# Optimization experiments

Hardware: AMD Instinct MI355X
Metric: run time of the kernel (lower is better)

The kernel has to match this reference:

```python
import jax, jax.numpy as jnp
import numpy as np

N, E = 100000, 1600000
IN, H, OUT = 64, 64, 32
BN_EPS = 1e-5


def setup_inputs() -> dict:
    key = jax.random.key(0)
    ks = jax.random.split(key, 13)

    def w(k, shape, fan_in):
        return jax.random.uniform(k, shape, jnp.float32, -1.0, 1.0) / np.sqrt(fan_in)

    return {
        "x": jax.random.normal(ks[0], (N, IN), jnp.float32),
        "edge_index": jax.random.randint(ks[1], (2, E), 0, N, jnp.int32),
        "W1": w(ks[2], (IN, H), IN),
        "b1": jnp.zeros((H,), jnp.float32),
        "gamma": jnp.ones((H,), jnp.float32),
        "beta": jnp.zeros((H,), jnp.float32),
        "W2": w(ks[3], (H, H), H),
        "b2": jnp.zeros((H,), jnp.float32),
        "lin2_w": w(ks[4], (H, OUT), H),
        "lin2_b": w(ks[5], (OUT,), H),
        "lin3_w": w(ks[6], (OUT, H), OUT),
        "lin3_b": w(ks[7], (H,), OUT),
    }


def gcn_conv(x, src, dst, W, b):
    # PyG GCNConv: h = D^{-1/2} (A + I) D^{-1/2} (x W) + b
    n = x.shape[0]
    h = x @ W  # [N, H]
    loop = jnp.arange(n, dtype=src.dtype)
    s = jnp.concatenate([src, loop])  # add self-loops
    d = jnp.concatenate([dst, loop])
    deg = jax.ops.segment_sum(jnp.ones_like(s, x.dtype), d, num_segments=n)
    dinv = jnp.where(deg > 0, jax.lax.rsqrt(deg), 0.0)
    norm = dinv[s] * dinv[d]  # [E+N]
    msg = h[s] * norm[:, None]  # gather + scale
    out = jax.ops.segment_sum(msg, d, num_segments=n)  # scatter-add
    return out + b


def reference(x, edge_index, W1, b1, gamma, beta, W2, b2, lin2_w, lin2_b, lin3_w, lin3_b):
    src, dst = edge_index[0], edge_index[1]
    h = gcn_conv(x, src, dst, W1, b1)
    # BatchNorm1d in eval mode with default running stats (mean=0, var=1)
    h = gamma * (h * jax.lax.rsqrt(jnp.float32(1.0 + BN_EPS))) + beta
    h = jax.nn.relu(h)  # dropout is identity in eval
    h = gcn_conv(h, src, dst, W2, b2)
    logits = h @ lin2_w + lin2_b  # [N, OUT]
    p = jax.nn.softmax(logits, axis=-1)
    ent = -jnp.sum(p * jnp.log(p + 1e-9), axis=-1)  # [N]
    wts = 1.0 / (ent + 1e-10)
    wts = (wts - wts.min()) / (wts.max() - wts.min())
    wts = jax.nn.softmax(wts, axis=0)  # [N]
    graph = jnp.sum(logits * wts[:, None], axis=0, keepdims=True)  # [1, OUT]
    return graph @ lin3_w + lin3_b  # [1, H]
```

## Files before the change

kernel.cpp:

```cpp
#include <hip/hip_runtime.h>
#include <hip/hip_bf16.h>
#include <hip/hip_fp8.h>
#include <math.h>


#define F 64
#define OUTF 32
#define PB 128
#define LEDGE 5632
#define WG 512
#define C1S 24
#define BN_INV 0.9999950000374997f
#define ESC_X 32.0f
#define IESC_X 0.03125f
#define ESC_Z 64.0f
#define IESC_Z 0.015625f

typedef short bf16x8 __attribute__((ext_vector_type(8)));
typedef float f32x4 __attribute__((ext_vector_type(4)));
typedef const __attribute__((address_space(1))) void* gas_ptr;
typedef __attribute__((address_space(3))) void* las_ptr;

__device__ __forceinline__ unsigned short f2bf(float f) {
    unsigned u = __float_as_uint(f);
    return (unsigned short)((u + 0x7fffu + ((u >> 16) & 1u)) >> 16);
}
__device__ __forceinline__ float bf2f(unsigned short h) {
    return __uint_as_float((unsigned)h << 16);
}

#if __has_builtin(__builtin_amdgcn_cvt_f32_fp8) && __has_builtin(__builtin_amdgcn_cvt_pk_fp8_f32)
__device__ __forceinline__ float4 fp8x4(unsigned v) {
    return make_float4(__builtin_amdgcn_cvt_f32_fp8((int)v, 0),
                       __builtin_amdgcn_cvt_f32_fp8((int)v, 1),
                       __builtin_amdgcn_cvt_f32_fp8((int)v, 2),
                       __builtin_amdgcn_cvt_f32_fp8((int)v, 3));
}
__device__ __forceinline__ unsigned fp8pk4(float a, float b, float c, float d) {
    int r = __builtin_amdgcn_cvt_pk_fp8_f32(a, b, 0, false);
    r = __builtin_amdgcn_cvt_pk_fp8_f32(c, d, r, true);
    return (unsigned)r;
}
__device__ __forceinline__ unsigned char fp8enc1(float a) {
    return (unsigned char)(__builtin_amdgcn_cvt_pk_fp8_f32(a, a, 0, false) & 0xff);
}
#else
__device__ __forceinline__ float fp8d1(unsigned char b) {
    __hip_fp8_e4m3 v; v.__x = (__hip_fp8_storage_t)b; return (float)v;
}
__device__ __forceinline__ float4 fp8x4(unsigned v) {
    return make_float4(fp8d1(v & 255u), fp8d1((v >> 8) & 255u), fp8d1((v >> 16) & 255u), fp8d1((v >> 24) & 255u));
}
__device__ __forceinline__ unsigned char fp8enc1(float a) {
    return (unsigned char)__hip_fp8_e4m3(a).__x;
}
__device__ __forceinline__ unsigned fp8pk4(float a, float b, float c, float d) {
    return (unsigned)fp8enc1(a) | ((unsigned)fp8enc1(b) << 8) | ((unsigned)fp8enc1(c) << 16) | ((unsigned)fp8enc1(d) << 24);
}
#endif

__device__ __forceinline__ void scan_btot(const int* __restrict__ btot, int* sbase, int NBK, int tid) {
    if (tid < 64) {
        int lane = tid;
        int vals[8];
        int lsum = 0;
#pragma unroll
        for (int q = 0; q < 8; q++) {
            int idx = lane * 8 + q;
            int v = (idx < NBK) ? btot[idx] : 0;
            vals[q] = lsum;
            lsum += v;
        }
        int run = lsum;
        for (int off = 1; off < 64; off <<= 1) {
            int u = __shfl_up(run, off, 64);
            if (lane >= off) run += u;
        }
        int excl = run - lsum;
#pragma unroll
        for (int q = 0; q < 8; q++) {
            int idx = lane * 8 + q;
            if (idx <= NBK) sbase[idx] = excl + vals[q];
        }
        if (lane == 63) sbase[NBK] = run;
    }
    __syncthreads();
}

__global__ __launch_bounds__(256) void k_hist(const int* __restrict__ dst, int* __restrict__ hist,
                                              int E, int NBK,
                                              const float* __restrict__ W1, const float* __restrict__ b1,
                                              const float* __restrict__ gamma, const float* __restrict__ beta,
                                              const float* __restrict__ W2, const float* __restrict__ b2,
                                              const float* __restrict__ l2w, const float* __restrict__ l2b,
                                              unsigned short* __restrict__ w1f, unsigned short* __restrict__ w2f,
                                              float* __restrict__ bias1f, float* __restrict__ b2l2) {
    __shared__ int lh[512];
    int t = threadIdx.x, blk = blockIdx.x;
    if (blk >= PB) {
        int tt = (blk - PB) * 256 + t;
        int k = tt >> 5, cc = tt & 31;
        float o = 0.0f;
        for (int j = 0; j < F; j++) o += W2[k * F + j] * l2w[j * OUTF + cc];
        {
            int t2 = cc >> 4, s = k >> 5, kb = (k >> 3) & 3, jj = k & 7;
            int ln = kb * 16 + (cc & 15);
            w2f[(size_t)((t2 * 2 + s) * 64 + ln) * 8 + jj] = f2bf(o);
        }
        for (int e = tt; e < F * F; e += 2048) {
            int kk = e >> 6, c = e & 63;
            float wv = W1[kk * F + c] * gamma[c] * BN_INV;
            int t1i = c >> 4, s = kk >> 5, kb = (kk >> 3) & 3, jj = kk & 7;
            int ln = kb * 16 + (c & 15);
            w1f[(size_t)((t1i * 2 + s) * 64 + ln) * 8 + jj] = f2bf(wv);
        }
        if (tt < F) bias1f[tt] = fmaf(b1[tt], gamma[tt] * BN_INV, beta[tt]);
        if (tt < OUTF) {
            float b = l2b[tt];
            for (int j = 0; j < F; j++) b += b2[j] * l2w[j * OUTF + tt];
            b2l2[tt] = b;
        }
        return;
    }
    for (int b = t; b < NBK; b += 256) lh[b] = 0;
    __syncthreads();
    int chunk = (E + PB - 1) / PB;
    int beg = blk * chunk, end = min(beg + chunk, E);
    for (int e = beg + t; e < end; e += 256) atomicAdd(&lh[dst[e] >> 8], 1);
    __syncthreads();
    for (int b = t; b < NBK; b += 256) hist[blk * NBK + b] = lh[b];
}

__global__ __launch_bounds__(PB) void k_hscan1(int* __restrict__ hist, int* __restrict__ btot, int NBK) {
    __shared__ int s[PB];
    int b = blockIdx.x, t = threadIdx.x;
    int v = hist[t * NBK + b];
    s[t] = v;
    __syncthreads();
    for (int off = 1; off < PB; off <<= 1) {
        int u = (t >= off) ? s[t - off] : 0;
        __syncthreads();
        s[t] += u;
        __syncthreads();
    }
    hist[t * NBK + b] = s[t] - v;
    if (t == PB - 1) btot[b] = s[t];
}

__global__ __launch_bounds__(256) void k_place(const int* __restrict__ src, const int* __restrict__ dst,
                                               const int* __restrict__ hist, const int* __restrict__ btot,
                                               unsigned* __restrict__ bucketArr, int E, int NBK) {
    __shared__ int cur[512];
    __shared__ int sbase[513];
    int t = threadIdx.x, blk = blockIdx.x;
    scan_btot(btot, sbase, NBK, t);
    for (int b = t; b < NBK; b += 256) cur[b] = hist[blk * NBK + b] + sbase[b];
    __syncthreads();
    int chunk = (E + PB - 1) / PB;
    int beg = blk * chunk, end = min(beg + chunk, E);
    for (int e = beg + t; e < end; e += 256) {
        int d = dst[e], sidx = src[e];
        int p = atomicAdd(&cur[d >> 8], 1);
        bucketArr[p] = ((unsigned)sidx << 8) | (unsigned)(d & 255);
    }
}

__global__ __launch_bounds__(256) void k_binsort(const unsigned* __restrict__ bucketArr,
                                                 const int* __restrict__ btot,
                                                 int* __restrict__ eidx, int4* __restrict__ meta,
                                                 const float4* __restrict__ x4, unsigned* __restrict__ xq, int N, int NBK) {
    __shared__ unsigned ledge[LEDGE];
    __shared__ int lcnt[256], lofs[256], lcur[256], lscan[256];
    __shared__ int sbase[513];
    __shared__ float ldinv[256];
    int b = blockIdx.x, t = threadIdx.x;
    scan_btot(btot, sbase, NBK, t);
    int gb = sbase[b];
    int count = min(sbase[b + 1] - gb, LEDGE);
    for (int j = t; j < count; j += 256) ledge[j] = bucketArr[gb + j];
    lcnt[t] = 0;
    __syncthreads();
    for (int j = t; j < count; j += 256) atomicAdd(&lcnt[ledge[j] & 255u], 1);
    __syncthreads();
    int deg = lcnt[t];
    lscan[t] = deg;
    __syncthreads();
    for (int off = 1; off < 256; off <<= 1) {
        int u = (t >= off) ? lscan[t - off] : 0;
        __syncthreads();
        lscan[t] += u;
        __syncthreads();
    }
    lofs[t] = lscan[t] - deg;
    lcur[t] = 0;
    int node = (b << 8) + t;
    float di = rsqrtf((float)deg + 1.0f);
    ldinv[t] = di;
    if (node < N) meta[node] = make_int4(gb + lofs[t], deg, __float_as_int(di), 0);
    __syncthreads();
    for (int j = t; j < count; j += 256) {
        unsigned v = ledge[j];
        int loc = (int)(v & 255u);
        int p = atomicAdd(&lcur[loc], 1);
        eidx[gb + lofs[loc] + p] = (int)(v >> 8);
    }
    for (int idx = t; idx < 256 * 16; idx += 256) {
        int nd = (b << 8) + (idx >> 4);
        if (nd < N) {
            float d2 = ldinv[idx >> 4] * ESC_X;
            float4 v = x4[(size_t)nd * 16 + (idx & 15)];
            xq[(size_t)nd * 16 + (idx & 15)] = fp8pk4(v.x * d2, v.y * d2, v.z * d2, v.w * d2);
        }
    }
}

__global__ __launch_bounds__(128) void k_c1z(const char* __restrict__ xqc,
                                             const int4* __restrict__ meta,
                                             const int* __restrict__ eidx,
                                             const unsigned short* __restrict__ w1f,
                                             const unsigned short* __restrict__ w2f,
                                             const float* __restrict__ bias1f,
                                             unsigned char* __restrict__ z2q, int N, int Em1) {
    __shared__ __align__(16) unsigned char stage[2][C1S][64 * 16];
    __shared__ __align__(16) unsigned short tile[2][16][72];
    __shared__ float ldin[2][16];
    int tid = threadIdx.x, wave = tid >> 6, lane = tid & 63;
    int g = lane >> 2, gl = lane & 3, gbase = lane & 60;
    int i = (blockIdx.x * 2 + wave) * 16 + g;
    int ic = min(i, N - 1);
    int4 m = meta[ic];
    int beg = m.x;
    int dcnt = (i < N) ? m.y : 0;
    float dis = __int_as_float(m.z) * IESC_X;
    if (gl == 0) ldin[wave][g] = __int_as_float(m.z);
    int s0 = eidx[min(beg + gl, Em1)];
    int s1 = eidx[min(beg + 4 + gl, Em1)];
    int s2 = eidx[min(beg + 8 + gl, Em1)];
    int s3 = eidx[min(beg + 12 + gl, Em1)];
    int s4 = eidx[min(beg + 16 + gl, Em1)];
    int s5 = eidx[min(beg + 20 + gl, Em1)];
    uint4 selfv = *(const uint4*)(xqc + (size_t)ic * 64 + gl * 16);
#pragma unroll
    for (int k = 0; k < C1S; k++) {
        int sreg = (k < 4) ? s0 : (k < 8) ? s1 : (k < 12) ? s2 : (k < 16) ? s3 : (k < 20) ? s4 : s5;
        int sv = __shfl(sreg, gbase + (k & 3), 64);
        if (k < dcnt) {
            const void* gp = xqc + (size_t)sv * 64 + gl * 16;
            __builtin_amdgcn_global_load_lds((gas_ptr)gp, (las_ptr)&stage[wave][k][0], 16, 0, 0);
        }
    }
    int cl = lane & 15, kb = lane >> 4;
    const bf16x8* w1v = (const bf16x8*)w1f;
    const bf16x8* w2v = (const bf16x8*)w2f;
    bf16x8 w1frag[8];
#pragma unroll
    for (int q = 0; q < 8; q++) w1frag[q] = w1v[q * 64 + lane];
    bf16x8 w2frag[4];
#pragma unroll
    for (int q = 0; q < 4; q++) w2frag[q] = w2v[q * 64 + lane];
    float bias_t[4];
#pragma unroll
    for (int t = 0; t < 4; t++) bias_t[t] = bias1f[t * 16 + cl];
    float4 a0 = fp8x4(selfv.x), a1 = fp8x4(selfv.y), a2 = fp8x4(selfv.z), a3 = fp8x4(selfv.w);
    asm volatile("s_waitcnt vmcnt(0)" ::: "memory");
#pragma unroll
    for (int k = 0; k < C1S; k++) {
        if (k < dcnt) {
            uint4 v = *(const uint4*)&stage[wave][k][lane * 16];
            float4 vA = fp8x4(v.x), vB = fp8x4(v.y), vC = fp8x4(v.z), vD = fp8x4(v.w);
            a0.x += vA.x; a0.y += vA.y; a0.z += vA.z; a0.w += vA.w;
            a1.x += vB.x; a1.y += vB.y; a1.z += vB.z; a1.w += vB.w;
            a2.x += vC.x; a2.y += vC.y; a2.z += vC.z; a2.w += vC.w;
            a3.x += vD.x; a3.y += vD.y; a3.z += vD.z; a3.w += vD.w;
        }
    }
    for (int base = C1S; base < dcnt; base += 4) {
        int j = base + gl;
        int ss = eidx[min(beg + j, Em1)];
        int cnt = min(dcnt - base, 4);
#pragma unroll
        for (int k = 0; k < 4; k++) {
            if (k < cnt) {
                int sv = __shfl(ss, gbase + k, 64);
                uint4 v = *(const uint4*)(xqc + (size_t)sv * 64 + gl * 16);
                float4 vA = fp8x4(v.x), vB = fp8x4(v.y), vC = fp8x4(v.z), vD = fp8x4(v.w);
                a0.x += vA.x; a0.y += vA.y; a0.z += vA.z; a0.w += vA.w;
                a1.x += vB.x; a1.y += vB.y; a1.z += vB.z; a1.w += vB.w;
                a2.x += vC.x; a2.y += vC.y; a2.z += vC.z; a2.w += vC.w;
                a3.x += vD.x; a3.y += vD.y; a3.z += vD.z; a3.w += vD.w;
            }
        }
    }
    {
        uint4 o1, o2;
        o1.x = (unsigned)f2bf(a0.x * dis) | ((unsigned)f2bf(a0.y * dis) << 16);
        o1.y = (unsigned)f2bf(a0.z * dis) | ((unsigned)f2bf(a0.w * dis) << 16);
        o1.z = (unsigned)f2bf(a1.x * dis) | ((unsigned)f2bf(a1.y * dis) << 16);
        o1.w = (unsigned)f2bf(a1.z * dis) | ((unsigned)f2bf(a1.w * dis) << 16);
        o2.x = (unsigned)f2bf(a2.x * dis) | ((unsigned)f2bf(a2.y * dis) << 16);
        o2.y = (unsigned)f2bf(a2.z * dis) | ((unsigned)f2bf(a2.w * dis) << 16);
        o2.z = (unsigned)f2bf(a3.x * dis) | ((unsigned)f2bf(a3.y * dis) << 16);
        o2.w = (unsigned)f2bf(a3.z * dis) | ((unsigned)f2bf(a3.w * dis) << 16);
        uint4* tp = (uint4*)&tile[wave][g][gl * 16];
        tp[0] = o1;
        tp[1] = o2;
    }
    bf16x8 af0 = *(const bf16x8*)&tile[wave][cl][kb * 8];
    bf16x8 af1 = *(const bf16x8*)&tile[wave][cl][32 + kb * 8];
    f32x4 acc[4] = {};
#pragma unroll
    for (int t = 0; t < 4; t++) {
        acc[t] = __builtin_amdgcn_mfma_f32_16x16x32_bf16(af0, w1frag[t * 2 + 0], acc[t], 0, 0, 0);
        acc[t] = __builtin_amdgcn_mfma_f32_16x16x32_bf16(af1, w1frag[t * 2 + 1], acc[t], 0, 0, 0);
    }
    float di[4];
#pragma unroll
    for (int j = 0; j < 4; j++) di[j] = ldin[wave][kb * 4 + j];
#pragma unroll
    for (int t = 0; t < 4; t++)
#pragma unroll
        for (int j = 0; j < 4; j++) {
            float h = fmaxf(acc[t][j] + bias_t[t], 0.0f) * di[j];
            tile[wave][kb * 4 + j][t * 16 + cl] = f2bf(h);
        }
    bf16x8 h0 = *(const bf16x8*)&tile[wave][cl][kb * 8];
    bf16x8 h1 = *(const bf16x8*)&tile[wave][cl][32 + kb * 8];
    f32x4 accz[2] = {};
#pragma unroll
    for (int t2 = 0; t2 < 2; t2++) {
        accz[t2] = __builtin_amdgcn_mfma_f32_16x16x32_bf16(h0, w2frag[t2 * 2 + 0], accz[t2], 0, 0, 0);
        accz[t2] = __builtin_amdgcn_mfma_f32_16x16x32_bf16(h1, w2frag[t2 * 2 + 1], accz[t2], 0, 0, 0);
    }
    int row0 = (blockIdx.x * 2 + wave) * 16;
#pragma unroll
    for (int t2 = 0; t2 < 2; t2++)
#pragma unroll
        for (int j = 0; j < 4; j++) {
            int r = row0 + kb * 4 + j;
            if (r < N) z2q[(size_t)r * OUTF + t2 * 16 + cl] = fp8enc1(accz[t2][j] * ESC_Z);
        }
}

__device__ __forceinline__ void conv2_consume(const uint2 (&vbuf)[24], uint2 selfv, int dcnt,
                                              int i, int beg, float dis, int gl, int gbase,
                                              const uint2* __restrict__ z2q2, const int* __restrict__ eidx,
                                              int Em1, float4 bvA, float4 bvB,
                                              unsigned short* __restrict__ logits_bf,
                                              float* __restrict__ wraw,
                                              float& mnW, float& mxW, int N) {
    float4 aA0 = fp8x4(selfv.x), aB0 = fp8x4(selfv.y);
    if (i >= N) { aA0 = make_float4(0.f, 0.f, 0.f, 0.f); aB0 = aA0; }
    float4 aA1 = make_float4(0.f, 0.f, 0.f, 0.f), aB1 = aA1;
#pragma unroll
    for (int k = 0; k < 24; k++) {
        if (k < dcnt) {
            float4 vA = fp8x4(vbuf[k].x), vB = fp8x4(vbuf[k].y);
            if (k & 1) {
                aA1.x += vA.x; aA1.y += vA.y; aA1.z += vA.z; aA1.w += vA.w;
                aB1.x += vB.x; aB1.y += vB.y; aB1.z += vB.z; aB1.w += vB.w;
            } else {
                aA0.x += vA.x; aA0.y += vA.y; aA0.z += vA.z; aA0.w += vA.w;
                aB0.x += vB.x; aB0.y += vB.y; aB0.z += vB.z; aB0.w += vB.w;
            }
        }
    }
    for (int base = 24; base < dcnt; base += 4) {
        int j = base + gl;
        int ss = eidx[min(beg + j, Em1)];
        int cnt = min(dcnt - base, 4);
#pragma unroll
        for (int k = 0; k < 4; k++) {
            if (k < cnt) {
                int sv = __shfl(ss, gbase + k, 64);
                uint2 v = z2q2[(size_t)sv * 4 + gl];
                float4 vA = fp8x4(v.x), vB = fp8x4(v.y);
                aA0.x += vA.x; aA0.y += vA.y; aA0.z += vA.z; aA0.w += vA.w;
                aB0.x += vB.x; aB0.y += vB.y; aB0.z += vB.z; aB0.w += vB.w;
            }
        }
    }
    float4 lgA, lgB;
    lgA.x = fmaf(aA0.x + aA1.x, dis, bvA.x);
    lgA.y = fmaf(aA0.y + aA1.y, dis, bvA.y);
    lgA.z = fmaf(aA0.z + aA1.z, dis, bvA.z);
    lgA.w = fmaf(aA0.w + aA1.w, dis, bvA.w);
    lgB.x = fmaf(aB0.x + aB1.x, dis, bvB.x);
    lgB.y = fmaf(aB0.y + aB1.y, dis, bvB.y);
    lgB.z = fmaf(aB0.z + aB1.z, dis, bvB.z);
    lgB.w = fmaf(aB0.w + aB1.w, dis, bvB.w);
    if (i < N) {
        uint4 ob;
        ob.x = (unsigned)f2bf(lgA.x) | ((unsigned)f2bf(lgA.y) << 16);
        ob.y = (unsigned)f2bf(lgA.z) | ((unsigned)f2bf(lgA.w) << 16);
        ob.z = (unsigned)f2bf(lgB.x) | ((unsigned)f2bf(lgB.y) << 16);
        ob.w = (unsigned)f2bf(lgB.z) | ((unsigned)f2bf(lgB.w) << 16);
        *(uint4*)(logits_bf + (size_t)i * OUTF + gl * 8) = ob;
    }
    float m8 = fmaxf(fmaxf(fmaxf(lgA.x, lgA.y), fmaxf(lgA.z, lgA.w)),
                     fmaxf(fmaxf(lgB.x, lgB.y), fmaxf(lgB.z, lgB.w)));
    for (int off = 2; off > 0; off >>= 1) m8 = fmaxf(m8, __shfl_xor(m8, off, 4));
    float p0 = __expf(lgA.x - m8), p1 = __expf(lgA.y - m8), p2 = __expf(lgA.z - m8), p3 = __expf(lgA.w - m8);
    float p4 = __expf(lgB.x - m8), p5 = __expf(lgB.y - m8), p6 = __expf(lgB.z - m8), p7 = __expf(lgB.w - m8);
    float s8 = p0 + p1 + p2 + p3 + p4 + p5 + p6 + p7;
    for (int off = 2; off > 0; off >>= 1) s8 += __shfl_xor(s8, off, 4);
    float inv = 1.0f / s8;
    float t0 = p0 * inv, t1v = p1 * inv, t2v = p2 * inv, t3 = p3 * inv;
    float t4 = p4 * inv, t5 = p5 * inv, t6 = p6 * inv, t7 = p7 * inv;
    float e8 = t0 * __logf(t0 + 1e-9f) + t1v * __logf(t1v + 1e-9f) + t2v * __logf(t2v + 1e-9f) + t3 * __logf(t3 + 1e-9f) +
               t4 * __logf(t4 + 1e-9f) + t5 * __logf(t5 + 1e-9f) + t6 * __logf(t6 + 1e-9f) + t7 * __logf(t7 + 1e-9f);
    for (int off = 2; off > 0; off >>= 1) e8 += __shfl_xor(e8, off, 4);
    float w = 1.0f / (-e8 + 1e-10f);
    if (i < N) {
        if (gl == 0) wraw[i] = w;
        mnW = fminf(mnW, w);
        mxW = fmaxf(mxW, w);
    }
}

__global__ __launch_bounds__(256, 2) void k_conv2agg(const uint2* __restrict__ z2q2,
                                                     const int4* __restrict__ meta,
                                                     const int* __restrict__ eidx, const float* __restrict__ b2l2,
                                                     unsigned short* __restrict__ logits_bf, float* __restrict__ wraw,
                                                     float* __restrict__ mnmx, int N, int Em1) {
    __shared__ float smn[4], smx[4];
    int tid = threadIdx.x, wave = tid >> 6, lane = tid & 63;
    int g = lane >> 2, gl = lane & 3, gbase = lane & 60;
    float4 bvA = ((const float4*)b2l2)[gl * 2];
    float4 bvB = ((const float4*)b2l2)[gl * 2 + 1];
    int wgid = blockIdx.x * 4 + wave;
    int i0 = wgid * 32 + g;
    int i1 = wgid * 32 + 16 + g;
    int i0c = min(i0, N - 1), i1c = min(i1, N - 1);
    int4 m0 = meta[i0c], m1 = meta[i1c];
    int beg0 = m0.x, beg1 = m1.x;
    int d0 = (i0 < N) ? m0.y : 0;
    int d1 = (i1 < N) ? m1.y : 0;
    float dis0 = __int_as_float(m0.z) * IESC_Z;
    float dis1 = __int_as_float(m1.z) * IESC_Z;
    int sA0 = eidx[min(beg0 + gl, Em1)];
    int sA1 = eidx[min(beg0 + 4 + gl, Em1)];
    int sA2 = eidx[min(beg0 + 8 + gl, Em1)];
    int sA3 = eidx[min(beg0 + 12 + gl, Em1)];
    int sA4 = eidx[min(beg0 + 16 + gl, Em1)];
    int sA5 = eidx[min(beg0 + 20 + gl, Em1)];
    int sB0 = eidx[min(beg1 + gl, Em1)];
    int sB1 = eidx[min(beg1 + 4 + gl, Em1)];
    int sB2 = eidx[min(beg1 + 8 + gl, Em1)];
    int sB3 = eidx[min(beg1 + 12 + gl, Em1)];
    int sB4 = eidx[min(beg1 + 16 + gl, Em1)];
    int sB5 = eidx[min(beg1 + 20 + gl, Em1)];
    uint2 self0 = z2q2[(size_t)i0c * 4 + gl];
    uint2 self1 = z2q2[(size_t)i1c * 4 + gl];
    uint2 vb0[24], vb1[24];
#pragma unroll
    for (int k = 0; k < 24; k++) {
        int sreg = (k < 4) ? sA0 : (k < 8) ? sA1 : (k < 12) ? sA2 : (k < 16) ? sA3 : (k < 20) ? sA4 : sA5;
        int sv = __shfl(sreg, gbase + (k & 3), 64);
        sv = (k < d0) ? sv : i0c;
        vb0[k] = z2q2[(size_t)sv * 4 + gl];
    }
#pragma unroll
    for (int k = 0; k < 24; k++) {
        int sreg = (k < 4) ? sB0 : (k < 8) ? sB1 : (k < 12) ? sB2 : (k < 16) ? sB3 : (k < 20) ? sB4 : sB5;
        int sv = __shfl(sreg, gbase + (k & 3), 64);
        sv = (k < d1) ? sv : i1c;
        vb1[k] = z2q2[(size_t)sv * 4 + gl];
    }
    __builtin_amdgcn_sched_barrier(0);
    float mnW = INFINITY, mxW = -INFINITY;
    conv2_consume(vb0, self0, d0, i0, beg0, dis0, gl, gbase, z2q2, eidx, Em1,
                  bvA, bvB, logits_bf, wraw, mnW, mxW, N);
    conv2_consume(vb1, self1, d1, i1, beg1, dis1, gl, gbase, z2q2, eidx, Em1,
                  bvA, bvB, logits_bf, wraw, mnW, mxW, N);
    for (int off = 32; off > 0; off >>= 1) {
        mnW = fminf(mnW, __shfl_xor(mnW, off, 64));
        mxW = fmaxf(mxW, __shfl_xor(mxW, off, 64));
    }
    if (lane == 0) { smn[wave] = mnW; smx[wave] = mxW; }
    __syncthreads();
    if (tid == 0) {
        mnmx[blockIdx.x * 2]     = fminf(fminf(smn[0], smn[1]), fminf(smn[2], smn[3]));
        mnmx[blockIdx.x * 2 + 1] = fmaxf(fmaxf(smx[0], smx[1]), fmaxf(smx[2], smx[3]));
    }
}

__global__ __launch_bounds__(256) void k_weight(const unsigned short* __restrict__ logits_bf,
                                                const float* __restrict__ wraw,
                                                const float* __restrict__ mnmx, int nmm,
                                                float* __restrict__ part, int N) {
    __shared__ float rmn[4], rmx[4];
    float mn = INFINITY, mx = -INFINITY;
    for (int j = threadIdx.x; j < nmm; j += 256) {
        mn = fminf(mn, mnmx[j * 2]);
        mx = fmaxf(mx, mnmx[j * 2 + 1]);
    }
    for (int off = 32; off > 0; off >>= 1) {
        mn = fminf(mn, __shfl_xor(mn, off, 64));
        mx = fmaxf(mx, __shfl_xor(mx, off, 64));
    }
    int wv = threadIdx.x >> 6;
    if ((threadIdx.x & 63) == 0) { rmn[wv] = mn; rmx[wv] = mx; }
    __syncthreads();
    mn = fminf(fminf(rmn[0], rmn[1]), fminf(rmn[2], rmn[3]));
    mx = fmaxf(fmaxf(rmx[0], rmx[1]), fmaxf(rmx[2], rmx[3]));
    float inv = 1.0f / (mx - mn);
    int c = threadIdx.x & 31;
    int g = threadIdx.x >> 5;
    float acc = 0.0f, es = 0.0f;
    for (int r = blockIdx.x * 8 + g; r < N; r += gridDim.x * 8) {
        float e = __expf((wraw[r] - mn) * inv);
        acc += e * bf2f(logits_bf[(size_t)r * OUTF + c]);
        if (c == 0) es += e;
    }
    __shared__ float sa[8][OUTF];
    __shared__ float se[8];
    sa[g][c] = acc;
    if (c == 0) se[g] = es;
    __syncthreads();
    if (g == 0) {
        float t = sa[0][c];
#pragma unroll
        for (int i = 1; i < 8; i++) t += sa[i][c];
        part[blockIdx.x * 36 + c] = t;
        if (c == 0) {
            float u = 0.0f;
#pragma unroll
            for (int i = 0; i < 8; i++) u += se[i];
            part[blockIdx.x * 36 + 32] = u;
        }
    }
}

__global__ __launch_bounds__(256) void k_final(const float* __restrict__ part,
                                               const float* __restrict__ w3, const float* __restrict__ b3,
                                               float* __restrict__ out) {
    __shared__ float sa[8][OUTF];
    __shared__ float se[8];
    __shared__ float facc[OUTF + 1];
    int tid = threadIdx.x;
    int g = tid >> 5, c = tid & 31;
    float acc = 0.0f, es = 0.0f;
    for (int p = g; p < WG; p += 8) {
        acc += part[p * 36 + c];
        if (c == 0) es += part[p * 36 + 32];
    }
    sa[g][c] = acc;
    if (c == 0) se[g] = es;
    __syncthreads();
    if (tid < OUTF) {
        float t = 0.0f;
#pragma unroll
        for (int i = 0; i < 8; i++) t += sa[i][tid];
        facc[tid] = t;
    }
    if (tid == 32) {
        float u = 0.0f;
#pragma unroll
        for (int i = 0; i < 8; i++) u += se[i];
        facc[OUTF] = u;
    }
    __syncthreads();
    if (tid < F) {
        float s = facc[OUTF];
        float o = b3[tid];
#pragma unroll
        for (int cc = 0; cc < OUTF; cc++) o += (facc[cc] / s) * w3[cc * F + tid];
        out[tid] = o;
    }
}

extern "C" void kernel_launch(void* const* d_in, const int* in_sizes, int n_in,
                              void* d_out, int out_size, void* d_ws, size_t ws_size,
                              hipStream_t stream) {
    const float* x     = (const float*)d_in[0];
    const int*   ei    = (const int*)d_in[1];
    const float* W1    = (const float*)d_in[2];
    const float* b1    = (const float*)d_in[3];
    const float* gamma = (const float*)d_in[4];
    const float* beta  = (const float*)d_in[5];
    const float* W2    = (const float*)d_in[6];
    const float* b2    = (const float*)d_in[7];
    const float* l2w   = (const float*)d_in[8];
    const float* l2b   = (const float*)d_in[9];
    const float* l3w   = (const float*)d_in[10];
    const float* l3b   = (const float*)d_in[11];

    int N = in_sizes[0] / F;
    int E = in_sizes[1] / 2;
    const int* src = ei;
    const int* dst = ei + E;
    int NBK = (N + 255) >> 8;

    char* p = (char*)d_ws;
    int* hist = (int*)p;                p += (size_t)PB * NBK * 4;
    int* btot = (int*)p;                p += 512 * 4;
    unsigned* bucketArr = (unsigned*)p; p += (size_t)E * 4;
    int4* meta = (int4*)p;              p += (size_t)N * 16;
    int* eidx = (int*)p;                p += (size_t)E * 4;
    float* mnmx = (float*)p;            p += 2048 * 4;
    float* part = (float*)p;            p += (size_t)WG * 36 * 4;
    unsigned short* w1f = (unsigned short*)p;  p += F * F * 2;
    unsigned short* w2f = (unsigned short*)p;  p += F * OUTF * 2;
    float* bias1f = (float*)p;          p += F * 4;
    float* b2l2 = (float*)p;            p += OUTF * 4 + 32;
    unsigned* xq = (unsigned*)p;        p += (size_t)N * F;
    unsigned char* z2q = (unsigned char*)p; p += (size_t)N * OUTF;
    unsigned short* logits_bf = (unsigned short*)p; p += (size_t)N * OUTF * 2;
    float* wraw = (float*)p;            p += (size_t)N * 4;

    k_hist<<<PB + 8, 256, 0, stream>>>(dst, hist, E, NBK, W1, b1, gamma, beta, W2, b2, l2w, l2b,
                                       w1f, w2f, bias1f, b2l2);
    k_hscan1<<<NBK, PB, 0, stream>>>(hist, btot, NBK);
    k_place<<<PB, 256, 0, stream>>>(src, dst, hist, btot, bucketArr, E, NBK);
    k_binsort<<<NBK, 256, 0, stream>>>(bucketArr, btot, eidx, meta, (const float4*)x, xq, N, NBK);

    int nb1 = (N + 31) / 32;
    k_c1z<<<nb1, 128, 0, stream>>>((const char*)xq, meta, eidx, w1f, w2f, bias1f, z2q, N, E - 1);
    int nt = (N + 15) >> 4;
    int wg2 = (nt + 1) >> 1;
    int nb2 = (wg2 + 3) >> 2;
    k_conv2agg<<<nb2, 256, 0, stream>>>((const uint2*)z2q, meta, eidx, b2l2, logits_bf, wraw, mnmx, N, E - 1);

    k_weight<<<WG, 256, 0, stream>>>(logits_bf, wraw, mnmx, nb2, part, N);
    k_final<<<1, 256, 0, stream>>>(part, l3w, l3b, (float*)d_out);
}
```

Baseline: 251.8 us.

## Split fused conv1+matmul kernel and narrow per-node lane groups for gathers

The fused conv1-aggregate-plus-MFMA kernel is split into a gather kernel (16 lanes per node, 4-byte loads into LDS) that writes bf16 aggregated features, and a separate MFMA kernel that computes relu(W1)·W2 into fp8 z. The conv2 aggregation is rewritten the same way (8 lanes per node, staged through LDS via global_load_lds instead of register prefetch of two nodes). Workspace buffers are aliased to reuse xq and t1 storage. The aim is more memory-level parallelism and occupancy in the gathers, at the cost of an extra kernel launch and a bf16 round-trip of the intermediate through global memory.

```diff
diff --git a/kernel.cpp b/kernel.cpp
--- a/kernel.cpp
+++ b/kernel.cpp
@@ -214,42 +214,81 @@
     }
 }
 
-__global__ __launch_bounds__(128) void k_c1z(const char* __restrict__ xqc,
-                                             const int4* __restrict__ meta,
-                                             const int* __restrict__ eidx,
-                                             const unsigned short* __restrict__ w1f,
-                                             const unsigned short* __restrict__ w2f,
-                                             const float* __restrict__ bias1f,
-                                             unsigned char* __restrict__ z2q, int N, int Em1) {
-    __shared__ __align__(16) unsigned char stage[2][C1S][64 * 16];
-    __shared__ __align__(16) unsigned short tile[2][16][72];
-    __shared__ float ldin[2][16];
+__global__ __launch_bounds__(256) void k_conv1s(const char* __restrict__ xqc,
+                                                const int4* __restrict__ meta,
+                                                const int* __restrict__ eidx,
+                                                unsigned short* __restrict__ t1, int N, int Em1) {
+    __shared__ __align__(16) unsigned char stage[4][C1S][256];
     int tid = threadIdx.x, wave = tid >> 6, lane = tid & 63;
-    int g = lane >> 2, gl = lane & 3, gbase = lane & 60;
-    int i = (blockIdx.x * 2 + wave) * 16 + g;
+    int g = lane >> 4, gl = lane & 15, gbase = lane & 48;
+    int i = (blockIdx.x * 4 + wave) * 4 + g;
     int ic = min(i, N - 1);
     int4 m = meta[ic];
     int beg = m.x;
     int dcnt = (i < N) ? m.y : 0;
     float dis = __int_as_float(m.z) * IESC_X;
-    if (gl == 0) ldin[wave][g] = __int_as_float(m.z);
     int s0 = eidx[min(beg + gl, Em1)];
-    int s1 = eidx[min(beg + 4 + gl, Em1)];
-    int s2 = eidx[min(beg + 8 + gl, Em1)];
-    int s3 = eidx[min(beg + 12 + gl, Em1)];
-    int s4 = eidx[min(beg + 16 + gl, Em1)];
-    int s5 = eidx[min(beg + 20 + gl, Em1)];
-    uint4 selfv = *(const uint4*)(xqc + (size_t)ic * 64 + gl * 16);
+    int s1 = eidx[min(beg + 16 + gl, Em1)];
+    unsigned selfv = *(const unsigned*)(xqc + (size_t)ic * 64 + gl * 4);
 #pragma unroll
     for (int k = 0; k < C1S; k++) {
-        int sreg = (k < 4) ? s0 : (k < 8) ? s1 : (k < 12) ? s2 : (k < 16) ? s3 : (k < 20) ? s4 : s5;
-        int sv = __shfl(sreg, gbase + (k & 3), 64);
+        int sreg = (k < 16) ? s0 : s1;
+        int sv = __shfl(sreg, gbase + (k & 15), 64);
         if (k < dcnt) {
-            const void* gp = xqc + (size_t)sv * 64 + gl * 16;
-            __builtin_amdgcn_global_load_lds((gas_ptr)gp, (las_ptr)&stage[wave][k][0], 16, 0, 0);
-        }
-    }
+            const void* gp = xqc + (size_t)sv * 64 + gl * 4;
+            __builtin_amdgcn_global_load_lds((gas_ptr)gp, (las_ptr)&stage[wave][k][0], 4, 0, 0);
+        }
+    }
+    float4 a = fp8x4(selfv);
+    asm volatile("s_waitcnt vmcnt(0)" ::: "memory");
+#pragma unroll
+    for (int k = 0; k < C1S; k++) {
+        if (k < dcnt) {
+            unsigned v = *(const unsigned*)&stage[wave][k][lane * 4];
+            float4 vv = fp8x4(v);
+            a.x += vv.x; a.y += vv.y; a.z += vv.z; a.w += vv.w;
+        }
+    }
+    for (int base = C1S; base < dcnt; base += 16) {
+        int j = base + gl;
+        int ss = eidx[min(beg + j, Em1)];
+        int cnt = min(dcnt - base, 16);
+        for (int k = 0; k < cnt; k++) {
+            int sv = __shfl(ss, gbase + k, 64);
+            unsigned v = *(const unsigned*)(xqc + (size_t)sv * 64 + gl * 4);
+            float4 vv = fp8x4(v);
+            a.x += vv.x; a.y += vv.y; a.z += vv.z; a.w += vv.w;
+        }
+    }
+    if (i < N) {
+        uint2 ob;
+        ob.x = (unsigned)f2bf(a.x * dis) | ((unsigned)f2bf(a.y * dis) << 16);
+        ob.y = (unsigned)f2bf(a.z * dis) | ((unsigned)f2bf(a.w * dis) << 16);
+        *(uint2*)(t1 + (size_t)i * F + gl * 4) = ob;
+    }
+}
+
+__global__ __launch_bounds__(256) void k_zm(const unsigned short* __restrict__ t1bf,
+                                            const int4* __restrict__ meta,
+                                            const unsigned short* __restrict__ w1f,
+                                            const unsigned short* __restrict__ w2f,
+                                            const float* __restrict__ bias1f,
+                                            unsigned char* __restrict__ z2q, int N) {
+    __shared__ __align__(16) unsigned short hlds[4][16][72];
+    __shared__ float ldin[4][16];
+    int tid = threadIdx.x, wave = tid >> 6, lane = tid & 63;
     int cl = lane & 15, kb = lane >> 4;
+    int ntiles = (N + 15) >> 4;
+    int tile = blockIdx.x * 4 + wave;
+    if (tile >= ntiles) return;
+    int row0 = tile << 4;
+
+    int ra = min(row0 + cl, N - 1);
+    const bf16x8* arow = (const bf16x8*)(t1bf + (size_t)ra * F);
+    bf16x8 a0 = arow[kb];
+    bf16x8 a1 = arow[4 + kb];
+    if (lane < 16) ldin[wave][lane] = __int_as_float(meta[min(row0 + lane, N - 1)].z);
+
     const bf16x8* w1v = (const bf16x8*)w1f;
     const bf16x8* w2v = (const bf16x8*)w2f;
     bf16x8 w1frag[8];
@@ -261,57 +300,12 @@
     float bias_t[4];
 #pragma unroll
     for (int t = 0; t < 4; t++) bias_t[t] = bias1f[t * 16 + cl];
-    float4 a0 = fp8x4(selfv.x), a1 = fp8x4(selfv.y), a2 = fp8x4(selfv.z), a3 = fp8x4(selfv.w);
-    asm volatile("s_waitcnt vmcnt(0)" ::: "memory");
-#pragma unroll
-    for (int k = 0; k < C1S; k++) {
-        if (k < dcnt) {
-            uint4 v = *(const uint4*)&stage[wave][k][lane * 16];
-            float4 vA = fp8x4(v.x), vB = fp8x4(v.y), vC = fp8x4(v.z), vD = fp8x4(v.w);
-            a0.x += vA.x; a0.y += vA.y; a0.z += vA.z; a0.w += vA.w;
-            a1.x += vB.x; a1.y += vB.y; a1.z += vB.z; a1.w += vB.w;
-            a2.x += vC.x; a2.y += vC.y; a2.z += vC.z; a2.w += vC.w;
-            a3.x += vD.x; a3.y += vD.y; a3.z += vD.z; a3.w += vD.w;
-        }
-    }
-    for (int base = C1S; base < dcnt; base += 4) {
-        int j = base + gl;
-        int ss = eidx[min(beg + j, Em1)];
-        int cnt = min(dcnt - base, 4);
-#pragma unroll
-        for (int k = 0; k < 4; k++) {
-            if (k < cnt) {
-                int sv = __shfl(ss, gbase + k, 64);
-                uint4 v = *(const uint4*)(xqc + (size_t)sv * 64 + gl * 16);
-                float4 vA = fp8x4(v.x), vB = fp8x4(v.y), vC = fp8x4(v.z), vD = fp8x4(v.w);
-                a0.x += vA.x; a0.y += vA.y; a0.z += vA.z; a0.w += vA.w;
-                a1.x += vB.x; a1.y += vB.y; a1.z += vB.z; a1.w += vB.w;
-                a2.x += vC.x; a2.y += vC.y; a2.z += vC.z; a2.w += vC.w;
-                a3.x += vD.x; a3.y += vD.y; a3.z += vD.z; a3.w += vD.w;
-            }
-        }
-    }
-    {
-        uint4 o1, o2;
-        o1.x = (unsigned)f2bf(a0.x * dis) | ((unsigned)f2bf(a0.y * dis) << 16);
-        o1.y = (unsigned)f2bf(a0.z * dis) | ((unsigned)f2bf(a0.w * dis) << 16);
-        o1.z = (unsigned)f2bf(a1.x * dis) | ((unsigned)f2bf(a1.y * dis) << 16);
-        o1.w = (unsigned)f2bf(a1.z * dis) | ((unsigned)f2bf(a1.w * dis) << 16);
-        o2.x = (unsigned)f2bf(a2.x * dis) | ((unsigned)f2bf(a2.y * dis) << 16);
-        o2.y = (unsigned)f2bf(a2.z * dis) | ((unsigned)f2bf(a2.w * dis) << 16);
-        o2.z = (unsigned)f2bf(a3.x * dis) | ((unsigned)f2bf(a3.y * dis) << 16);
-        o2.w = (unsigned)f2bf(a3.z * dis) | ((unsigned)f2bf(a3.w * dis) << 16);
-        uint4* tp = (uint4*)&tile[wave][g][gl * 16];
-        tp[0] = o1;
-        tp[1] = o2;
-    }
-    bf16x8 af0 = *(const bf16x8*)&tile[wave][cl][kb * 8];
-    bf16x8 af1 = *(const bf16x8*)&tile[wave][cl][32 + kb * 8];
+
     f32x4 acc[4] = {};
 #pragma unroll
     for (int t = 0; t < 4; t++) {
-        acc[t] = __builtin_amdgcn_mfma_f32_16x16x32_bf16(af0, w1frag[t * 2 + 0], acc[t], 0, 0, 0);
-        acc[t] = __builtin_amdgcn_mfma_f32_16x16x32_bf16(af1, w1frag[t * 2 + 1], acc[t], 0, 0, 0);
+        acc[t] = __builtin_amdgcn_mfma_f32_16x16x32_bf16(a0, w1frag[t * 2 + 0], acc[t], 0, 0, 0);
+        acc[t] = __builtin_amdgcn_mfma_f32_16x16x32_bf16(a1, w1frag[t * 2 + 1], acc[t], 0, 0, 0);
     }
     float di[4];
 #pragma unroll
@@ -321,17 +315,16 @@
 #pragma unroll
         for (int j = 0; j < 4; j++) {
             float h = fmaxf(acc[t][j] + bias_t[t], 0.0f) * di[j];
-            tile[wave][kb * 4 + j][t * 16 + cl] = f2bf(h);
-        }
-    bf16x8 h0 = *(const bf16x8*)&tile[wave][cl][kb * 8];
-    bf16x8 h1 = *(const bf16x8*)&tile[wave][cl][32 + kb * 8];
+            hlds[wave][kb * 4 + j][t * 16 + cl] = f2bf(h);
+        }
+    bf16x8 h0 = *(const bf16x8*)&hlds[wave][cl][kb * 8];
+    bf16x8 h1 = *(const bf16x8*)&hlds[wave][cl][32 + kb * 8];
     f32x4 accz[2] = {};
 #pragma unroll
     for (int t2 = 0; t2 < 2; t2++) {
         accz[t2] = __builtin_amdgcn_mfma_f32_16x16x32_bf16(h0, w2frag[t2 * 2 + 0], accz[t2], 0, 0, 0);
         accz[t2] = __builtin_amdgcn_mfma_f32_16x16x32_bf16(h1, w2frag[t2 * 2 + 1], accz[t2], 0, 0, 0);
     }
-    int row0 = (blockIdx.x * 2 + wave) * 16;
 #pragma unroll
     for (int t2 = 0; t2 < 2; t2++)
 #pragma unroll
@@ -341,137 +334,85 @@
         }
 }
 
-__device__ __forceinline__ void conv2_consume(const uint2 (&vbuf)[24], uint2 selfv, int dcnt,
-                                              int i, int beg, float dis, int gl, int gbase,
-                                              const uint2* __restrict__ z2q2, const int* __restrict__ eidx,
-                                              int Em1, float4 bvA, float4 bvB,
-                                              unsigned short* __restrict__ logits_bf,
-                                              float* __restrict__ wraw,
-                                              float& mnW, float& mxW, int N) {
-    float4 aA0 = fp8x4(selfv.x), aB0 = fp8x4(selfv.y);
-    if (i >= N) { aA0 = make_float4(0.f, 0.f, 0.f, 0.f); aB0 = aA0; }
-    float4 aA1 = make_float4(0.f, 0.f, 0.f, 0.f), aB1 = aA1;
-#pragma unroll
-    for (int k = 0; k < 24; k++) {
+__global__ __launch_bounds__(256) void k_conv2s(const char* __restrict__ z2qc,
+                                                const int4* __restrict__ meta,
+                                                const int* __restrict__ eidx, const float* __restrict__ b2l2,
+                                                unsigned short* __restrict__ logits_bf, float* __restrict__ wraw,
+                                                float* __restrict__ mnmx, int N, int Em1) {
+    __shared__ __align__(16) unsigned char stage[4][C1S][256];
+    __shared__ float smn[4], smx[4];
+    int tid = threadIdx.x, wave = tid >> 6, lane = tid & 63;
+    int g = lane >> 3, gl = lane & 7, gbase = lane & 56;
+    int i = (blockIdx.x * 4 + wave) * 8 + g;
+    int ic = min(i, N - 1);
+    int4 m = meta[ic];
+    int beg = m.x;
+    int dcnt = (i < N) ? m.y : 0;
+    float dis = __int_as_float(m.z) * IESC_Z;
+    int s0 = eidx[min(beg + gl, Em1)];
+    int s1 = eidx[min(beg + 8 + gl, Em1)];
+    int s2 = eidx[min(beg + 16 + gl, Em1)];
+    unsigned selfv = *(const unsigned*)(z2qc + (size_t)ic * 32 + gl * 4);
+#pragma unroll
+    for (int k = 0; k < C1S; k++) {
+        int sreg = (k < 8) ? s0 : (k < 16) ? s1 : s2;
+        int sv = __shfl(sreg, gbase + (k & 7), 64);
         if (k < dcnt) {
-            float4 vA = fp8x4(vbuf[k].x), vB = fp8x4(vbuf[k].y);
-            if (k & 1) {
-                aA1.x += vA.x; aA1.y += vA.y; aA1.z += vA.z; aA1.w += vA.w;
-                aB1.x += vB.x; aB1.y += vB.y; aB1.z += vB.z; aB1.w += vB.w;
-            } else {
-                aA0.x += vA.x; aA0.y += vA.y; aA0.z += vA.z; aA0.w += vA.w;
-                aB0.x += vB.x; aB0.y += vB.y; aB0.z += vB.z; aB0.w += vB.w;
-            }
-        }
-    }
-    for (int base = 24; base < dcnt; base += 4) {
+            const void* gp = z2qc + (size_t)sv * 32 + gl * 4;
+            __builtin_amdgcn_global_load_lds((gas_ptr)gp, (las_ptr)&stage[wave][k][0], 4, 0, 0);
+        }
+    }
+    float4 a = fp8x4(selfv);
+    if (i >= N) a = make_float4(0.f, 0.f, 0.f, 0.f);
+    asm volatile("s_waitcnt vmcnt(0)" ::: "memory");
+#pragma unroll
+    for (int k = 0; k < C1S; k++) {
+        if (k < dcnt) {
+            unsigned v = *(const unsigned*)&stage[wave][k][lane * 4];
+            float4 vv = fp8x4(v);
+            a.x += vv.x; a.y += vv.y; a.z += vv.z; a.w += vv.w;
+        }
+    }
+    for (int base = C1S; base < dcnt; base += 8) {
         int j = base + gl;
         int ss = eidx[min(beg + j, Em1)];
-        int cnt = min(dcnt - base, 4);
-#pragma unroll
-        for (int k = 0; k < 4; k++) {
-            if (k < cnt) {
-                int sv = __shfl(ss, gbase + k, 64);
-                uint2 v = z2q2[(size_t)sv * 4 + gl];
-                float4 vA = fp8x4(v.x), vB = fp8x4(v.y);
-                aA0.x += vA.x; aA0.y += vA.y; aA0.z += vA.z; aA0.w += vA.w;
-                aB0.x += vB.x; aB0.y += vB.y; aB0.z += vB.z; aB0.w += vB.w;
-            }
-        }
-    }
-    float4 lgA, lgB;
-    lgA.x = fmaf(aA0.x + aA1.x, dis, bvA.x);
-    lgA.y = fmaf(aA0.y + aA1.y, dis, bvA.y);
-    lgA.z = fmaf(aA0.z + aA1.z, dis, bvA.z);
-    lgA.w = fmaf(aA0.w + aA1.w, dis, bvA.w);
-    lgB.x = fmaf(aB0.x + aB1.x, dis, bvB.x);
-    lgB.y = fmaf(aB0.y + aB1.y, dis, bvB.y);
-    lgB.z = fmaf(aB0.z + aB1.z, dis, bvB.z);
-    lgB.w = fmaf(aB0.w + aB1.w, dis, bvB.w);
+        int cnt = min(dcnt - base, 8);
+        for (int k = 0; k < cnt; k++) {
+            int sv = __shfl(ss, gbase + k, 64);
+            unsigned v = *(const unsigned*)(z2qc + (size_t)sv * 32 + gl * 4);
+            float4 vv = fp8x4(v);
+            a.x += vv.x; a.y += vv.y; a.z += vv.z; a.w += vv.w;
+        }
+    }
+    float4 bv = ((const float4*)b2l2)[gl];
+    float4 lg;
+    lg.x = fmaf(a.x, dis, bv.x);
+    lg.y = fmaf(a.y, dis, bv.y);
+    lg.z = fmaf(a.z, dis, bv.z);
+    lg.w = fmaf(a.w, dis, bv.w);
     if (i < N) {
-        uint4 ob;
-        ob.x = (unsigned)f2bf(lgA.x) | ((unsigned)f2bf(lgA.y) << 16);
-        ob.y = (unsigned)f2bf(lgA.z) | ((unsigned)f2bf(lgA.w) << 16);
-        ob.z = (unsigned)f2bf(lgB.x) | ((unsigned)f2bf(lgB.y) << 16);
-        ob.w = (unsigned)f2bf(lgB.z) | ((unsigned)f2bf(lgB.w) << 16);
-        *(uint4*)(logits_bf + (size_t)i * OUTF + gl * 8) = ob;
-    }
-    float m8 = fmaxf(fmaxf(fmaxf(lgA.x, lgA.y), fmaxf(lgA.z, lgA.w)),
-                     fmaxf(fmaxf(lgB.x, lgB.y), fmaxf(lgB.z, lgB.w)));
-    for (int off = 2; off > 0; off >>= 1) m8 = fmaxf(m8, __shfl_xor(m8, off, 4));
-    float p0 = __expf(lgA.x - m8), p1 = __expf(lgA.y - m8), p2 = __expf(lgA.z - m8), p3 = __expf(lgA.w - m8);
-    float p4 = __expf(lgB.x - m8), p5 = __expf(lgB.y - m8), p6 = __expf(lgB.z - m8), p7 = __expf(lgB.w - m8);
-    float s8 = p0 + p1 + p2 + p3 + p4 + p5 + p6 + p7;
-    for (int off = 2; off > 0; off >>= 1) s8 += __shfl_xor(s8, off, 4);
+        uint2 ob;
+        ob.x = (unsigned)f2bf(lg.x) | ((unsigned)f2bf(lg.y) << 16);
+        ob.y = (unsigned)f2bf(lg.z) | ((unsigned)f2bf(lg.w) << 16);
+        *(uint2*)(logits_bf + (size_t)i * OUTF + gl * 4) = ob;
+    }
+    float m8 = fmaxf(fmaxf(lg.x, lg.y), fmaxf(lg.z, lg.w));
+    for (int off = 4; off > 0; off >>= 1) m8 = fmaxf(m8, __shfl_xor(m8, off, 8));
+    float p0 = __expf(lg.x - m8), p1 = __expf(lg.y - m8), p2 = __expf(lg.z - m8), p3 = __expf(lg.w - m8);
+    float s8 = p0 + p1 + p2 + p3;
+    for (int off = 4; off > 0; off >>= 1) s8 += __shfl_xor(s8, off, 8);
     float inv = 1.0f / s8;
     float t0 = p0 * inv, t1v = p1 * inv, t2v = p2 * inv, t3 = p3 * inv;
-    float t4 = p4 * inv, t5 = p5 * inv, t6 = p6 * inv, t7 = p7 * inv;
-    float e8 = t0 * __logf(t0 + 1e-9f) + t1v * __logf(t1v + 1e-9f) + t2v * __logf(t2v + 1e-9f) + t3 * __logf(t3 + 1e-9f) +
-               t4 * __logf(t4 + 1e-9f) + t5 * __logf(t5 + 1e-9f) + t6 * __logf(t6 + 1e-9f) + t7 * __logf(t7 + 1e-9f);
-    for (int off = 2; off > 0; off >>= 1) e8 += __shfl_xor(e8, off, 4);
+    float e8 = t0 * __logf(t0 + 1e-9f) + t1v * __logf(t1v + 1e-9f) +
+               t2v * __logf(t2v + 1e-9f) + t3 * __logf(t3 + 1e-9f);
+    for (int off = 4; off > 0; off >>= 1) e8 += __shfl_xor(e8, off, 8);
     float w = 1.0f / (-e8 + 1e-10f);
+    float mnW = INFINITY, mxW = -INFINITY;
     if (i < N) {
         if (gl == 0) wraw[i] = w;
-        mnW = fminf(mnW, w);
-        mxW = fmaxf(mxW, w);
-    }
-}
-
-__global__ __launch_bounds__(256, 2) void k_conv2agg(const uint2* __restrict__ z2q2,
-                                                     const int4* __restrict__ meta,
-                                                     const int* __restrict__ eidx, const float* __restrict__ b2l2,
-                                                     unsigned short* __restrict__ logits_bf, float* __restrict__ wraw,
-                                                     float* __restrict__ mnmx, int N, int Em1) {
-    __shared__ float smn[4], smx[4];
-    int tid = threadIdx.x, wave = tid >> 6, lane = tid & 63;
-    int g = lane >> 2, gl = lane & 3, gbase = lane & 60;
-    float4 bvA = ((const float4*)b2l2)[gl * 2];
-    float4 bvB = ((const float4*)b2l2)[gl * 2 + 1];
-    int wgid = blockIdx.x * 4 + wave;
-    int i0 = wgid * 32 + g;
-    int i1 = wgid * 32 + 16 + g;
-    int i0c = min(i0, N - 1), i1c = min(i1, N - 1);
-    int4 m0 = meta[i0c], m1 = meta[i1c];
-    int beg0 = m0.x, beg1 = m1.x;
-    int d0 = (i0 < N) ? m0.y : 0;
-    int d1 = (i1 < N) ? m1.y : 0;
-    float dis0 = __int_as_float(m0.z) * IESC_Z;
-    float dis1 = __int_as_float(m1.z) * IESC_Z;
-    int sA0 = eidx[min(beg0 + gl, Em1)];
-    int sA1 = eidx[min(beg0 + 4 + gl, Em1)];
-    int sA2 = eidx[min(beg0 + 8 + gl, Em1)];
-    int sA3 = eidx[min(beg0 + 12 + gl, Em1)];
-    int sA4 = eidx[min(beg0 + 16 + gl, Em1)];
-    int sA5 = eidx[min(beg0 + 20 + gl, Em1)];
-    int sB0 = eidx[min(beg1 + gl, Em1)];
-    int sB1 = eidx[min(beg1 + 4 + gl, Em1)];
-    int sB2 = eidx[min(beg1 + 8 + gl, Em1)];
-    int sB3 = eidx[min(beg1 + 12 + gl, Em1)];
-    int sB4 = eidx[min(beg1 + 16 + gl, Em1)];
-    int sB5 = eidx[min(beg1 + 20 + gl, Em1)];
-    uint2 self0 = z2q2[(size_t)i0c * 4 + gl];
-    uint2 self1 = z2q2[(size_t)i1c * 4 + gl];
-    uint2 vb0[24], vb1[24];
-#pragma unroll
-    for (int k = 0; k < 24; k++) {
-        int sreg = (k < 4) ? sA0 : (k < 8) ? sA1 : (k < 12) ? sA2 : (k < 16) ? sA3 : (k < 20) ? sA4 : sA5;
-        int sv = __shfl(sreg, gbase + (k & 3), 64);
-        sv = (k < d0) ? sv : i0c;
-        vb0[k] = z2q2[(size_t)sv * 4 + gl];
-    }
-#pragma unroll
-    for (int k = 0; k < 24; k++) {
-        int sreg = (k < 4) ? sB0 : (k < 8) ? sB1 : (k < 12) ? sB2 : (k < 16) ? sB3 : (k < 20) ? sB4 : sB5;
-        int sv = __shfl(sreg, gbase + (k & 3), 64);
-        sv = (k < d1) ? sv : i1c;
-        vb1[k] = z2q2[(size_t)sv * 4 + gl];
-    }
-    __builtin_amdgcn_sched_barrier(0);
-    float mnW = INFINITY, mxW = -INFINITY;
-    conv2_consume(vb0, self0, d0, i0, beg0, dis0, gl, gbase, z2q2, eidx, Em1,
-                  bvA, bvB, logits_bf, wraw, mnW, mxW, N);
-    conv2_consume(vb1, self1, d1, i1, beg1, dis1, gl, gbase, z2q2, eidx, Em1,
-                  bvA, bvB, logits_bf, wraw, mnW, mxW, N);
+        mnW = w;
+        mxW = w;
+    }
     for (int off = 32; off > 0; off >>= 1) {
         mnW = fminf(mnW, __shfl_xor(mnW, off, 64));
         mxW = fmaxf(mxW, __shfl_xor(mxW, off, 64));
@@ -597,16 +538,17 @@
     unsigned* bucketArr = (unsigned*)p; p += (size_t)E * 4;
     int4* meta = (int4*)p;              p += (size_t)N * 16;
     int* eidx = (int*)p;                p += (size_t)E * 4;
-    float* mnmx = (float*)p;            p += 2048 * 4;
+    float* mnmx = (float*)p;            p += 8192 * 4;
     float* part = (float*)p;            p += (size_t)WG * 36 * 4;
     unsigned short* w1f = (unsigned short*)p;  p += F * F * 2;
     unsigned short* w2f = (unsigned short*)p;  p += F * OUTF * 2;
     float* bias1f = (float*)p;          p += F * 4;
     float* b2l2 = (float*)p;            p += OUTF * 4 + 32;
     unsigned* xq = (unsigned*)p;        p += (size_t)N * F;
-    unsigned char* z2q = (unsigned char*)p; p += (size_t)N * OUTF;
-    unsigned short* logits_bf = (unsigned short*)p; p += (size_t)N * OUTF * 2;
+    unsigned short* t1bf = (unsigned short*)p; p += (size_t)N * F * 2;
     float* wraw = (float*)p;            p += (size_t)N * 4;
+    unsigned char* z2q = (unsigned char*)xq;
+    unsigned short* logits_bf = (unsigned short*)t1bf;
 
     k_hist<<<PB + 8, 256, 0, stream>>>(dst, hist, E, NBK, W1, b1, gamma, beta, W2, b2, l2w, l2b,
                                        w1f, w2f, bias1f, b2l2);
@@ -614,12 +556,12 @@
     k_place<<<PB, 256, 0, stream>>>(src, dst, hist, btot, bucketArr, E, NBK);
     k_binsort<<<NBK, 256, 0, stream>>>(bucketArr, btot, eidx, meta, (const float4*)x, xq, N, NBK);
 
-    int nb1 = (N + 31) / 32;
-    k_c1z<<<nb1, 128, 0, stream>>>((const char*)xq, meta, eidx, w1f, w2f, bias1f, z2q, N, E - 1);
+    int nb1 = (N + 15) / 16;
+    k_conv1s<<<nb1, 256, 0, stream>>>((const char*)xq, meta, eidx, t1bf, N, E - 1);
     int nt = (N + 15) >> 4;
-    int wg2 = (nt + 1) >> 1;
-    int nb2 = (wg2 + 3) >> 2;
-    k_conv2agg<<<nb2, 256, 0, stream>>>((const uint2*)z2q, meta, eidx, b2l2, logits_bf, wraw, mnmx, N, E - 1);
+    k_zm<<<(nt + 3) / 4, 256, 0, stream>>>(t1bf, meta, w1f, w2f, bias1f, z2q, N);
+    int nb2 = (N + 31) / 32;
+    k_conv2s<<<nb2, 256, 0, stream>>>((const char*)z2q, meta, eidx, b2l2, logits_bf, wraw, mnmx, N, E - 1);
 
     k_weight<<<WG, 256, 0, stream>>>(logits_bf, wraw, mnmx, nb2, part, N);
     k_final<<<1, 256, 0, stream>>>(part, l3w, l3b, (float*)d_out);
```

Result: faster. 243.7 us (-3.2%).
